# Optimization experiments

Measured on AMD Instinct MI355X. Metric: run time of the kernel, lower is better.

Reference implementation:

```python
import jax, jax.numpy as jnp
import numpy as np

# Structure constants T[k, p, q] = sign such that (a (x) b)_k = sum_{p,q} T[k,p,q] a_p b_q,
# transcribed term-by-term from clifford_product_3d (Cl(3,0), metric +,+,+).
_TERMS = [
    (0,0,0, 1),(0,1,1, 1),(0,2,2, 1),(0,3,3, 1),(0,4,4,-1),(0,5,5,-1),(0,6,6,-1),(0,7,7,-1),
    (1,0,1, 1),(1,1,0, 1),(1,2,4,-1),(1,3,5, 1),(1,4,2, 1),(1,5,3,-1),(1,6,7,-1),(1,7,6,-1),
    (2,0,2, 1),(2,1,4, 1),(2,2,0, 1),(2,3,6,-1),(2,4,1,-1),(2,5,7, 1),(2,6,3, 1),(2,7,5,-1),
    (3,0,3, 1),(3,1,5,-1),(3,2,6, 1),(3,3,0, 1),(3,4,7,-1),(3,5,1,-1),(3,6,2,-1),(3,7,4, 1),
    (4,0,4, 1),(4,1,2, 1),(4,2,1,-1),(4,3,7, 1),(4,4,0, 1),(4,5,6,-1),(4,6,5, 1),(4,7,3,-1),
    (5,0,5, 1),(5,1,3,-1),(5,2,7, 1),(5,3,1, 1),(5,4,6, 1),(5,5,0, 1),(5,6,4,-1),(5,7,2,-1),
    (6,0,6, 1),(6,1,7,-1),(6,2,3,-1),(6,3,2, 1),(6,4,5,-1),(6,5,4, 1),(6,6,0, 1),(6,7,1, 1),
    (7,0,7, 1),(7,1,6, 1),(7,2,5,-1),(7,3,4, 1),(7,4,3, 1),(7,5,2,-1),(7,6,1, 1),(7,7,0, 1),
]

def _clifford_table():
    T = np.zeros((8, 8, 8), dtype=np.float32)
    for k, p, q, s in _TERMS:
        T[k, p, q] = s
    return jnp.asarray(T)

_T = _clifford_table()


def setup_inputs() -> dict:
    key = jax.random.key(0)
    k1, k2 = jax.random.split(key)
    C_in, C_out = 8, 8
    x = jax.random.normal(k1, (4096, 512, C_in, 8), dtype=jnp.float32)
    weight = jax.random.normal(k2, (C_out, C_in, 8), dtype=jnp.float32) * C_in ** (-0.5)
    bias = jnp.zeros((C_out, 8), dtype=jnp.float32)
    return {"x": x, "weight": weight, "bias": bias}


def reference(x, weight, bias):
    # out[..., o, k] = sum_i sum_{p,q} T[k,p,q] * weight[o,i,p] * x[..., i, q] + bias[o,k]
    # Contract weight with T first (tiny), then a single GEMM-like contraction over (i,q):
    # avoids the naive [..., C_out, C_in, 8] broadcast intermediate entirely.
    wT = jnp.einsum('kpq,oip->oikq', _T.astype(weight.dtype), weight)  # [C_out, C_in, 8, 8]
    out = jnp.einsum('oikq,biq->bok', wT, x.reshape(-1, *x.shape[-2:]))
    out = out.reshape(*x.shape[:-2], *out.shape[-2:])
    return out + bias
```

## Files before the change

kernel.cpp:

```cpp
#include <hip/hip_runtime.h>
#include <hip/hip_bf16.h>
#include <stdint.h>

__constant__ signed char QTAB[64] = {
    0,1,2,3,4,5,6,7,
    1,0,4,5,2,3,7,6,
    2,4,0,6,1,7,3,5,
    3,5,6,0,7,1,2,4,
    4,2,1,7,0,6,5,3,
    5,3,7,1,6,0,4,2,
    6,7,3,2,5,4,0,1,
    7,6,5,4,3,2,1,0};
__constant__ signed char SGN[64] = {
    1, 1, 1, 1,-1,-1,-1,-1,
    1, 1,-1, 1, 1,-1,-1,-1,
    1, 1, 1,-1,-1, 1, 1,-1,
    1,-1, 1, 1,-1,-1,-1, 1,
    1, 1,-1, 1, 1,-1, 1,-1,
    1,-1, 1, 1, 1, 1,-1,-1,
    1,-1,-1, 1,-1, 1, 1, 1,
    1, 1,-1, 1, 1,-1, 1, 1};

typedef __attribute__((ext_vector_type(8))) short bf16x8;
typedef __attribute__((ext_vector_type(4))) float f32x4;
typedef __attribute__((ext_vector_type(4))) unsigned int u32x4;
typedef __attribute__((address_space(1))) const float gfloat;
typedef __attribute__((address_space(3))) float sfloat;

#define SBAR __builtin_amdgcn_sched_barrier(0)
#define WAITVM(N)                                         \
    asm volatile("s_waitcnt vmcnt(" #N ")" ::: "memory"); \
    SBAR

__global__ void clifford_prep(const float* __restrict__ weight,
                              float* __restrict__ W2,
                              unsigned short* __restrict__ W2T) {
    int t = threadIdx.x;
    for (int e = t; e < 4096; e += 256) {
        int o = e >> 9, i = (e >> 6) & 7, k = (e >> 3) & 7, p = e & 7;
        int q = (int)QTAB[k * 8 + p];
        float s = (float)SGN[k * 8 + p];
        W2[((i * 8 + q) * 64) + (o * 8 + k)] = s * weight[(o * 8 + i) * 8 + p];
    }
    __syncthreads();
    for (int e = t; e < 4096; e += 256) {
        int n = e >> 6, k = e & 63;
        __hip_bfloat16 h = __float2bfloat16(W2[k * 64 + n]);
        W2T[n * 64 + k] = *reinterpret_cast<unsigned short*>(&h);
    }
}

static __device__ __forceinline__ short f2bf(float f) {
    __hip_bfloat16 h = __float2bfloat16(f);
    return *reinterpret_cast<short*>(&h);
}

#define ISSUE_CHUNK(CI, BP)                                                  \
    {                                                                        \
        const float* base_ = x + (size_t)(CI) * 2048;                        \
        _Pragma("unroll") for (int i_ = 0; i_ < 8; ++i_) {                   \
            int r_ = i_ * 4 + (l >> 4);                                      \
            const float* src_ =                                              \
                base_ + r_ * 64 + (((l & 15) ^ (r_ & 15)) << 2);             \
            __builtin_amdgcn_global_load_lds(                                \
                (gfloat*)src_, (sfloat*)((BP) + i_ * 256 + (l << 2)), 16, 0, \
                0);                                                          \
        }                                                                    \
    }

#define COMPUTE(BP)                                                          \
    {                                                                        \
        _Pragma("unroll") for (int kh = 0; kh < 2; ++kh) {                   \
            bf16x8 afr[2];                                                   \
            _Pragma("unroll") for (int mt = 0; mt < 2; ++mt) {               \
                int r_ = mt * 16 + (l & 15);                                 \
                int qa = kh * 8 + 2 * (l >> 4);                              \
                float4 lo = *(const float4*)((BP) + r_ * 64 +                \
                                             ((qa ^ (r_ & 15)) << 2));       \
                float4 hi = *(const float4*)((BP) + r_ * 64 +                \
                                             (((qa + 1) ^ (r_ & 15)) << 2)); \
                bf16x8 a_;                                                   \
                a_[0] = f2bf(lo.x); a_[1] = f2bf(lo.y);                      \
                a_[2] = f2bf(lo.z); a_[3] = f2bf(lo.w);                      \
                a_[4] = f2bf(hi.x); a_[5] = f2bf(hi.y);                      \
                a_[6] = f2bf(hi.z); a_[7] = f2bf(hi.w);                      \
                afr[mt] = a_;                                                \
            }                                                                \
            _Pragma("unroll") for (int nt = 0; nt < 4; ++nt) {               \
                int n_ = nt * 16 + (l & 15);                                 \
                int qb = kh * 4 + (l >> 4);                                  \
                bf16x8 bfr = *(const bf16x8*)((const char*)w2t + n_ * 128 +  \
                                              (((qb ^ (n_ & 7))) << 4));     \
                acc[0][nt] = __builtin_amdgcn_mfma_f32_16x16x32_bf16(        \
                    afr[0], bfr, acc[0][nt], 0, 0, 0);                       \
                acc[1][nt] = __builtin_amdgcn_mfma_f32_16x16x32_bf16(        \
                    afr[1], bfr, acc[1][nt], 0, 0, 0);                       \
            }                                                                \
        }                                                                    \
    }

#define STORE_CHUNK(CI, BP)                                                  \
    {                                                                        \
        _Pragma("unroll") for (int mt = 0; mt < 2; ++mt)                     \
        _Pragma("unroll") for (int nt = 0; nt < 4; ++nt)                     \
        _Pragma("unroll") for (int rg = 0; rg < 4; ++rg) {                   \
            int row_ = mt * 16 + 4 * (l >> 4) + rg;                          \
            (BP)[row_ * 64 + nt * 16 + (l & 15)] = acc[mt][nt][rg];          \
        }                                                                    \
        float* ob_ = out + (size_t)(CI) * 2048;                              \
        _Pragma("unroll") for (int j_ = 0; j_ < 8; ++j_) {                   \
            float4 v_ = *(const float4*)((BP) + j_ * 256 + (l << 2));        \
            *(float4*)(ob_ + j_ * 256 + (l << 2)) = v_;                      \
        }                                                                    \
    }

#define ACC_INIT                                                 \
    f32x4 acc[2][4];                                             \
    _Pragma("unroll") for (int mt = 0; mt < 2; ++mt)             \
    _Pragma("unroll") for (int nt = 0; nt < 4; ++nt) {           \
        acc[mt][nt][0] = bvv[nt]; acc[mt][nt][1] = bvv[nt];      \
        acc[mt][nt][2] = bvv[nt]; acc[mt][nt][3] = bvv[nt];      \
    }

__global__ __launch_bounds__(256) void clifford_main(
    const float* __restrict__ x, const unsigned short* __restrict__ W2T,
    const float* __restrict__ bias, float* __restrict__ out, int nB) {
    __shared__ __align__(16) float xbuf[4][2][2048];
    __shared__ __align__(16) unsigned short w2t[4096];

    const int tid = threadIdx.x;
    const int l = tid & 63;
    const int wv = tid >> 6;

#pragma unroll
    for (int gg = 0; gg < 2; ++gg) {
        int g = tid * 2 + gg;
        int n = g >> 3, q = g & 7;
        u32x4 v = *(const u32x4*)(W2T + n * 64 + q * 8);
        *(u32x4*)((char*)w2t + n * 128 + ((q ^ (n & 7)) << 4)) = v;
    }
    __syncthreads();

    float* xb0 = xbuf[wv][0];
    float* xb1 = xbuf[wv][1];
    const int nC = nB >> 5;
    const long long nW = (long long)gridDim.x * 4;
    const long long w = (long long)blockIdx.x * 4 + wv;
    const int cpw = (int)(nC / nW);
    const long long rem = nC - (long long)cpw * nW;

    float bvv[4];
#pragma unroll
    for (int nt = 0; nt < 4; ++nt) bvv[nt] = bias[nt * 16 + (l & 15)];
#pragma unroll
    for (int nt = 0; nt < 4; ++nt) asm volatile("" : "+v"(bvv[nt]));

    const long long c0 = w * cpw;
    if (cpw >= 3) {
        ISSUE_CHUNK(c0, xb0);
        ISSUE_CHUNK(c0 + 1, xb1);
        WAITVM(8);
        for (int i = 0; i < cpw - 2; ++i) {
            float* bp = (i & 1) ? xb1 : xb0;
            const long long c = c0 + i;
            ACC_INIT;
            COMPUTE(bp);
            STORE_CHUNK(c, bp);
            SBAR;
            ISSUE_CHUNK(c + 2, bp);
            WAITVM(16);
        }
        {
            float* bp = ((cpw - 2) & 1) ? xb1 : xb0;
            ACC_INIT;
            COMPUTE(bp);
            STORE_CHUNK(c0 + cpw - 2, bp);
            SBAR;
            WAITVM(8);
        }
        {
            float* bp = ((cpw - 1) & 1) ? xb1 : xb0;
            ACC_INIT;
            COMPUTE(bp);
            STORE_CHUNK(c0 + cpw - 1, bp);
        }
    } else {
        for (int i = 0; i < cpw; ++i) {
            ISSUE_CHUNK(c0 + i, xb0);
            WAITVM(0);
            ACC_INIT;
            COMPUTE(xb0);
            STORE_CHUNK(c0 + i, xb0);
            WAITVM(0);
        }
    }
    if (w < rem) {
        const long long c = nW * cpw + w;
        WAITVM(0);
        ISSUE_CHUNK(c, xb0);
        WAITVM(0);
        ACC_INIT;
        COMPUTE(xb0);
        STORE_CHUNK(c, xb0);
    }
}

extern "C" void kernel_launch(void* const* d_in, const int* in_sizes, int n_in,
                              void* d_out, int out_size, void* d_ws,
                              size_t ws_size, hipStream_t stream) {
    const float* x = (const float*)d_in[0];
    const float* weight = (const float*)d_in[1];
    const float* bias = (const float*)d_in[2];
    float* out = (float*)d_out;
    float* W2 = (float*)d_ws;
    unsigned short* W2T = (unsigned short*)(W2 + 4096);

    int nB = in_sizes[0] / 64;

    hipLaunchKernelGGL(clifford_prep, dim3(1), dim3(256), 0, stream, weight,
                       W2, W2T);
    int nC = nB >> 5;
    int blocks = 2048;
    if (blocks * 4 > nC) blocks = (nC + 3) / 4;
    if (blocks < 1) blocks = 1;
    hipLaunchKernelGGL(clifford_main, dim3(blocks), dim3(256), 0, stream, x,
                       W2T, bias, out, nB);
}
```

Measured before the change: 221.5 us.

## Halve per-wave chunk to 16 rows and store accumulators directly to global

Each wave now processes 16-row chunks instead of 32, halving LDS staging buffers and accumulator registers. Output is written straight from the MFMA accumulator registers to global memory, skipping the LDS round-trip used for coalesced float4 stores. The stores become scalar 4-byte writes with a strided per-lane pattern, which may cost write bandwidth. The vmcnt thresholds are adjusted to count these additional store instructions, and an lgkmcnt wait is added before the LDS buffer is reused.

New measurement: 231.7 us. 4.6% more time.

```diff
diff --git a/kernel.cpp b/kernel.cpp
--- a/kernel.cpp
+++ b/kernel.cpp
@@ -31,6 +31,9 @@
 #define WAITVM(N)                                         \
     asm volatile("s_waitcnt vmcnt(" #N ")" ::: "memory"); \
     SBAR
+#define WLGKM                                             \
+    asm volatile("s_waitcnt lgkmcnt(0)" ::: "memory");    \
+    SBAR
 
 __global__ void clifford_prep(const float* __restrict__ weight,
                               float* __restrict__ W2,
@@ -57,8 +60,8 @@
 
 #define ISSUE_CHUNK(CI, BP)                                                  \
     {                                                                        \
-        const float* base_ = x + (size_t)(CI) * 2048;                        \
-        _Pragma("unroll") for (int i_ = 0; i_ < 8; ++i_) {                   \
+        const float* base_ = x + (size_t)(CI) * 1024;                        \
+        _Pragma("unroll") for (int i_ = 0; i_ < 4; ++i_) {                   \
             int r_ = i_ * 4 + (l >> 4);                                      \
             const float* src_ =                                              \
                 base_ + r_ * 64 + (((l & 15) ^ (r_ & 15)) << 2);             \
@@ -71,61 +74,49 @@
 #define COMPUTE(BP)                                                          \
     {                                                                        \
         _Pragma("unroll") for (int kh = 0; kh < 2; ++kh) {                   \
-            bf16x8 afr[2];                                                   \
-            _Pragma("unroll") for (int mt = 0; mt < 2; ++mt) {               \
-                int r_ = mt * 16 + (l & 15);                                 \
-                int qa = kh * 8 + 2 * (l >> 4);                              \
-                float4 lo = *(const float4*)((BP) + r_ * 64 +                \
-                                             ((qa ^ (r_ & 15)) << 2));       \
-                float4 hi = *(const float4*)((BP) + r_ * 64 +                \
-                                             (((qa + 1) ^ (r_ & 15)) << 2)); \
-                bf16x8 a_;                                                   \
-                a_[0] = f2bf(lo.x); a_[1] = f2bf(lo.y);                      \
-                a_[2] = f2bf(lo.z); a_[3] = f2bf(lo.w);                      \
-                a_[4] = f2bf(hi.x); a_[5] = f2bf(hi.y);                      \
-                a_[6] = f2bf(hi.z); a_[7] = f2bf(hi.w);                      \
-                afr[mt] = a_;                                                \
-            }                                                                \
+            int r_ = (l & 15);                                               \
+            int qa = kh * 8 + 2 * (l >> 4);                                  \
+            float4 lo = *(const float4*)((BP) + r_ * 64 +                    \
+                                         ((qa ^ r_) << 2));                  \
+            float4 hi = *(const float4*)((BP) + r_ * 64 +                    \
+                                         (((qa + 1) ^ r_) << 2));            \
+            bf16x8 a_;                                                       \
+            a_[0] = f2bf(lo.x); a_[1] = f2bf(lo.y);                          \
+            a_[2] = f2bf(lo.z); a_[3] = f2bf(lo.w);                          \
+            a_[4] = f2bf(hi.x); a_[5] = f2bf(hi.y);                          \
+            a_[6] = f2bf(hi.z); a_[7] = f2bf(hi.w);                          \
             _Pragma("unroll") for (int nt = 0; nt < 4; ++nt) {               \
                 int n_ = nt * 16 + (l & 15);                                 \
                 int qb = kh * 4 + (l >> 4);                                  \
                 bf16x8 bfr = *(const bf16x8*)((const char*)w2t + n_ * 128 +  \
                                               (((qb ^ (n_ & 7))) << 4));     \
-                acc[0][nt] = __builtin_amdgcn_mfma_f32_16x16x32_bf16(        \
-                    afr[0], bfr, acc[0][nt], 0, 0, 0);                       \
-                acc[1][nt] = __builtin_amdgcn_mfma_f32_16x16x32_bf16(        \
-                    afr[1], bfr, acc[1][nt], 0, 0, 0);                       \
+                acc[nt] = __builtin_amdgcn_mfma_f32_16x16x32_bf16(           \
+                    a_, bfr, acc[nt], 0, 0, 0);                              \
             }                                                                \
         }                                                                    \
     }
 
-#define STORE_CHUNK(CI, BP)                                                  \
+#define STORE_CHUNK(CI)                                                      \
     {                                                                        \
-        _Pragma("unroll") for (int mt = 0; mt < 2; ++mt)                     \
+        float* ob_ = out + (size_t)(CI) * 1024;                              \
         _Pragma("unroll") for (int nt = 0; nt < 4; ++nt)                     \
         _Pragma("unroll") for (int rg = 0; rg < 4; ++rg) {                   \
-            int row_ = mt * 16 + 4 * (l >> 4) + rg;                          \
-            (BP)[row_ * 64 + nt * 16 + (l & 15)] = acc[mt][nt][rg];          \
+            int row_ = 4 * (l >> 4) + rg;                                    \
+            ob_[row_ * 64 + nt * 16 + (l & 15)] = acc[nt][rg];               \
         }                                                                    \
-        float* ob_ = out + (size_t)(CI) * 2048;                              \
-        _Pragma("unroll") for (int j_ = 0; j_ < 8; ++j_) {                   \
-            float4 v_ = *(const float4*)((BP) + j_ * 256 + (l << 2));        \
-            *(float4*)(ob_ + j_ * 256 + (l << 2)) = v_;                      \
-        }                                                                    \
-    }
-
-#define ACC_INIT                                                 \
-    f32x4 acc[2][4];                                             \
-    _Pragma("unroll") for (int mt = 0; mt < 2; ++mt)             \
-    _Pragma("unroll") for (int nt = 0; nt < 4; ++nt) {           \
-        acc[mt][nt][0] = bvv[nt]; acc[mt][nt][1] = bvv[nt];      \
-        acc[mt][nt][2] = bvv[nt]; acc[mt][nt][3] = bvv[nt];      \
+    }
+
+#define ACC_INIT                                                  \
+    f32x4 acc[4];                                                 \
+    _Pragma("unroll") for (int nt = 0; nt < 4; ++nt) {            \
+        acc[nt][0] = bvv[nt]; acc[nt][1] = bvv[nt];               \
+        acc[nt][2] = bvv[nt]; acc[nt][3] = bvv[nt];               \
     }
 
 __global__ __launch_bounds__(256) void clifford_main(
     const float* __restrict__ x, const unsigned short* __restrict__ W2T,
     const float* __restrict__ bias, float* __restrict__ out, int nB) {
-    __shared__ __align__(16) float xbuf[4][2][2048];
+    __shared__ __align__(16) float xbuf[4][2][1024];
     __shared__ __align__(16) unsigned short w2t[4096];
 
     const int tid = threadIdx.x;
@@ -143,7 +134,7 @@
 
     float* xb0 = xbuf[wv][0];
     float* xb1 = xbuf[wv][1];
-    const int nC = nB >> 5;
+    const int nC = nB >> 4;
     const long long nW = (long long)gridDim.x * 4;
     const long long w = (long long)blockIdx.x * 4 + wv;
     const int cpw = (int)(nC / nW);
@@ -159,30 +150,29 @@
     if (cpw >= 3) {
         ISSUE_CHUNK(c0, xb0);
         ISSUE_CHUNK(c0 + 1, xb1);
-        WAITVM(8);
+        WAITVM(4);
         for (int i = 0; i < cpw - 2; ++i) {
             float* bp = (i & 1) ? xb1 : xb0;
             const long long c = c0 + i;
             ACC_INIT;
             COMPUTE(bp);
-            STORE_CHUNK(c, bp);
-            SBAR;
+            STORE_CHUNK(c);
+            WLGKM;
             ISSUE_CHUNK(c + 2, bp);
-            WAITVM(16);
+            WAITVM(20);
         }
         {
             float* bp = ((cpw - 2) & 1) ? xb1 : xb0;
             ACC_INIT;
             COMPUTE(bp);
-            STORE_CHUNK(c0 + cpw - 2, bp);
-            SBAR;
-            WAITVM(8);
+            STORE_CHUNK(c0 + cpw - 2);
+            WAITVM(4);
         }
         {
             float* bp = ((cpw - 1) & 1) ? xb1 : xb0;
             ACC_INIT;
             COMPUTE(bp);
-            STORE_CHUNK(c0 + cpw - 1, bp);
+            STORE_CHUNK(c0 + cpw - 1);
         }
     } else {
         for (int i = 0; i < cpw; ++i) {
@@ -190,7 +180,8 @@
             WAITVM(0);
             ACC_INIT;
             COMPUTE(xb0);
-            STORE_CHUNK(c0 + i, xb0);
+            STORE_CHUNK(c0 + i);
+            WLGKM;
             WAITVM(0);
         }
     }
@@ -201,7 +192,7 @@
         WAITVM(0);
         ACC_INIT;
         COMPUTE(xb0);
-        STORE_CHUNK(c, xb0);
+        STORE_CHUNK(c);
     }
 }
 
@@ -219,7 +210,7 @@
 
     hipLaunchKernelGGL(clifford_prep, dim3(1), dim3(256), 0, stream, weight,
                        W2, W2T);
-    int nC = nB >> 5;
+    int nC = nB >> 4;
     int blocks = 2048;
     if (blocks * 4 > nC) blocks = (nC + 3) / 4;
     if (blocks < 1) blocks = 1;
```
